# Kernel tuning notes

Measured on AMD Instinct MI355X. Metric: run time of the kernel, lower is better.

## Reference

```python
import jax, jax.numpy as jnp
import numpy as np

LAYERS, H = 12, 8
MH1, MW1 = 32, 32
MH2, MW2 = 63, 63
LENGTHS = [616, 616, 616, 616, 608]  # 2 pairs + tail, sum = L
L = sum(LENGTHS)
N_WITHIN = MH1 * MW1
N_ACROSS = MH2 * MW2
ZERO_SLOT = N_WITHIN + N_ACROSS  # extra table entry that is always 0


def _build_index_maps():
    """Replicates set_indices/_compute_indices/_compute_masks with numpy (static ints)."""
    rng = np.random.default_rng(0)
    rows = rng.integers(0, 31, size=L)
    cols = rng.integers(0, 31, size=L)
    hc2, wc2 = (MH2 - 1) // 2, (MW2 - 1) // 2
    comb = np.full((L, L), ZERO_SLOT, dtype=np.int32)  # untouched cells read 0

    def within_block(r, c):
        hd = np.clip(r[None, :] - r[:, None], 0, MH1 - 1)
        wd = np.clip(c[None, :] - c[:, None], 0, MW1 - 1)
        return (hd * MW1 + wd).astype(np.int32)

    cur = 0
    npairs = len(LENGTHS) // 2
    for i in range(npairs):
        lx, ly = LENGTHS[2 * i], LENGTHS[2 * i + 1]
        xs, xe = cur, cur + lx
        ys, ye = xe, xe + ly
        xr, xc = rows[xs:xe], cols[xs:xe]
        yr, yc = rows[ys:ye], cols[ys:ye]
        comb[xs:xe, xs:xe] = within_block(xr, xc)
        comb[ys:ye, ys:ye] = within_block(yr, yc)
        hdxy = np.clip(yr[:, None] - xr[None, :] + hc2, 0, MH2 - 1)
        wdxy = np.clip(yc[:, None] - xc[None, :] + wc2, 0, MW2 - 1)
        comb[ys:ye, xs:xe] = N_WITHIN + (hdxy * MW2 + wdxy).astype(np.int32)
        cur = ye
    if len(LENGTHS) % 2 == 1:  # tail segment
        lx = LENGTHS[-1]
        xs, xe = cur, cur + lx
        comb[xs:xe, xs:xe] = within_block(rows[xs:xe], cols[xs:xe])

    special = rows == 0
    sp_mask = special[None, :] | special[:, None]
    causal = np.triu(np.ones((L, L), dtype=bool), 1)
    return comb, sp_mask, causal


def setup_inputs() -> dict:
    comb, sp_mask, causal = _build_index_maps()
    key = jax.random.key(0)
    k1, k2 = jax.random.split(key)
    within_bias = jax.random.normal(k1, (LAYERS, H, MH1, MW1), dtype=jnp.float32)
    across_bias = jax.random.normal(k2, (LAYERS, H, MH2, MW2), dtype=jnp.float32)
    return {
        "within_bias": within_bias,
        "across_bias": across_bias,
        "comb_idx": jnp.asarray(comb),
        "sp_mask": jnp.asarray(sp_mask),
        "causal": jnp.asarray(causal),
        "layer_idx": 3,
    }


def reference(within_bias, across_bias, comb_idx, sp_mask, causal, layer_idx):
    h = within_bias.shape[1]
    w = within_bias[layer_idx].reshape(h, -1)           # [H, mh1*mw1]
    a = across_bias[layer_idx].reshape(h, -1)           # [H, mh2*mw2]
    zero = jnp.zeros((h, 1), dtype=w.dtype)
    table = jnp.concatenate([w, a, zero], axis=1)       # [H, nw+na+1]
    attn = table[:, comb_idx]                           # [H, L, L] single gather
    neg = jnp.finfo(attn.dtype).min
    attn = jnp.where(sp_mask, jnp.zeros((), attn.dtype), attn)
    attn = jnp.where(causal, neg, attn)
    return attn[None]                                   # [1, H, L, L]
```

## Files before the change

### kernel.cpp

```cpp
#include <hip/hip_runtime.h>


constexpr int L  = 3072;
constexpr int H  = 8;
constexpr int NW = 32 * 32;
constexpr int NA = 63 * 63;
constexpr int ZERO_SLOT = NW + NA;
constexpr int TBL = ZERO_SLOT + 1;
constexpr unsigned short NEG_F16 = 0xFBFF;
constexpr size_t SPC_OFF = 79936;

typedef __attribute__((ext_vector_type(8))) short short8;

__device__ __forceinline__ unsigned short f16_safe(unsigned short v) {
    return (((v >> 10) & 0x1Fu) == 0x1Fu) ? (unsigned short)0 : v;
}

__global__ __launch_bounds__(256) void mga_prep(
    const unsigned short* __restrict__ within,
    const unsigned short* __restrict__ across,
    const int* __restrict__ layer_idx,
    const unsigned char* __restrict__ sp,
    unsigned short* __restrict__ tbl,
    unsigned char* __restrict__ spc)
{
    const int lw = layer_idx[0];
    const int layer = (lw >= 0 && lw < 12) ? lw : 3;
    const unsigned short* wbase = within + (size_t)layer * H * NW;
    const unsigned short* abase = across + (size_t)layer * H * NA;

    const int t = blockIdx.x * blockDim.x + threadIdx.x;
    if (t < TBL) {
        short8 v;
        #pragma unroll
        for (int h = 0; h < H; ++h) {
            unsigned short x;
            if (t < NW)             x = f16_safe(wbase[h * NW + t]);
            else if (t < ZERO_SLOT) x = f16_safe(abase[h * NA + (t - NW)]);
            else                    x = 0;
            v[h] = (short)x;
        }
        *reinterpret_cast<short8*>(tbl + (size_t)t * H) = v;
    }
    if (t < L) spc[t] = sp[(size_t)t * (L + 1)];
}

__global__ __launch_bounds__(256) void mga_gather(
    const unsigned short* __restrict__ tbl,
    const unsigned char* __restrict__ spc,
    const int*   __restrict__ comb,
    unsigned short* __restrict__ out)
{
    short8 cneg;
    #pragma unroll
    for (int k = 0; k < 8; ++k) cneg[k] = (short)NEG_F16;

    const int g  = blockIdx.x * blockDim.x + threadIdx.x;
    const int e0 = g * 8;
    const int i  = e0 / L;
    const int j  = e0 - i * L;

    unsigned short* o = out + e0;
    if (j > i) {
        #pragma unroll
        for (int h = 0; h < H; ++h)
            *reinterpret_cast<short8*>(o + (size_t)h * (L * L)) = cneg;
        return;
    }

    const int4 ia = *reinterpret_cast<const int4*>(comb + e0);
    const int4 ib = *reinterpret_cast<const int4*>(comb + e0 + 4);
    const unsigned long long spj =
        *reinterpret_cast<const unsigned long long*>(spc + j);
    const bool spi = spc[i] != 0;
    const int idxs[8] = {ia.x, ia.y, ia.z, ia.w, ib.x, ib.y, ib.z, ib.w};

    short8 tt[8];
    bool zm[8], nm[8];
    #pragma unroll
    for (int k = 0; k < 8; ++k) {
        unsigned int idx = (unsigned int)idxs[k];
        idx = (idx > (unsigned)ZERO_SLOT) ? (unsigned)ZERO_SLOT : idx;
        tt[k] = *reinterpret_cast<const short8*>(tbl + (size_t)idx * H);
        zm[k] = spi || (((spj >> (8 * k)) & 1ull) != 0ull);
        nm[k] = (j + k) > i;
    }

    #pragma unroll
    for (int h = 0; h < H; ++h) {
        short8 v;
        #pragma unroll
        for (int k = 0; k < 8; ++k) {
            const unsigned short t =
                nm[k] ? NEG_F16
                      : (zm[k] ? (unsigned short)0 : (unsigned short)tt[k][h]);
            v[k] = (short)t;
        }
        *reinterpret_cast<short8*>(o + (size_t)h * (L * L)) = v;
    }
}

__global__ __launch_bounds__(256) void mga_direct(
    const unsigned short* __restrict__ within,
    const unsigned short* __restrict__ across,
    const int*   __restrict__ comb,
    const unsigned char* __restrict__ sp,
    const int*   __restrict__ layer_idx,
    unsigned short* __restrict__ out)
{
    const int lw = layer_idx[0];
    const int layer = (lw >= 0 && lw < 12) ? lw : 3;
    const unsigned short* wbase = within + (size_t)layer * H * NW;
    const unsigned short* abase = across + (size_t)layer * H * NA;

    const int total  = (L * L) / 8;
    const int stride = gridDim.x * blockDim.x;
    for (int g = blockIdx.x * blockDim.x + threadIdx.x; g < total; g += stride) {
        const int e0 = g * 8;
        const int i  = e0 / L;
        const int j  = e0 - i * L;
        const int4 ia = *reinterpret_cast<const int4*>(comb + e0);
        const int4 ib = *reinterpret_cast<const int4*>(comb + e0 + 4);
        const unsigned long long sp8 =
            *reinterpret_cast<const unsigned long long*>(sp + e0);
        const int idxs[8] = {ia.x, ia.y, ia.z, ia.w, ib.x, ib.y, ib.z, ib.w};
        const unsigned short* p[8];
        int hs[8]; bool zm[8], nm[8];
        #pragma unroll
        for (int k = 0; k < 8; ++k) {
            int idx = idxs[k];
            if (idx < 0 || idx > ZERO_SLOT) idx = ZERO_SLOT;
            const bool isz = (idx >= ZERO_SLOT);
            const bool isw = (idx < NW);
            const unsigned short* pk = isw ? (wbase + idx) : (abase + (idx - NW));
            p[k]  = isz ? wbase : pk;
            hs[k] = isw ? NW : NA;
            zm[k] = isz || (((sp8 >> (8 * k)) & 1ull) != 0ull);
            nm[k] = (j + k) > i;
        }
        unsigned short* o = out + e0;
        #pragma unroll
        for (int h = 0; h < H; ++h) {
            short8 v;
            #pragma unroll
            for (int k = 0; k < 8; ++k) {
                unsigned short t;
                if (nm[k])      t = NEG_F16;
                else if (zm[k]) t = 0;
                else            t = f16_safe(p[k][h * hs[k]]);
                v[k] = (short)t;
            }
            *reinterpret_cast<short8*>(o + (size_t)h * (L * L)) = v;
        }
    }
}

extern "C" void kernel_launch(void* const* d_in, const int* in_sizes, int n_in,
                              void* d_out, int out_size, void* d_ws, size_t ws_size,
                              hipStream_t stream) {
    const unsigned short* within = (const unsigned short*)d_in[0];
    const unsigned short* across = (const unsigned short*)d_in[1];
    const int*   comb   = (const int*)d_in[2];
    const unsigned char* sp = (const unsigned char*)d_in[3];
    const int*   layer  = (const int*)d_in[5];
    unsigned short* out = (unsigned short*)d_out;

    if (ws_size >= SPC_OFF + L) {
        unsigned short* tbl = (unsigned short*)d_ws;
        unsigned char*  spc = (unsigned char*)d_ws + SPC_OFF;
        hipLaunchKernelGGL(mga_prep, dim3((TBL + 255) / 256), dim3(256),
                           0, stream, within, across, layer, sp, tbl, spc);
        hipLaunchKernelGGL(mga_gather, dim3((L * L / 8) / 256), dim3(256),
                           0, stream, tbl, spc, comb, out);
    } else {
        hipLaunchKernelGGL(mga_direct, dim3(2048), dim3(256), 0, stream,
                           within, across, comb, sp, layer, out);
    }
}
```

Measured before the change: 35.00 us.

## Split causal fill into prep kernel and gather only lower-triangle groups

Moves the writing of the strictly-upper-triangle NEG fill into the prep kernel, whose launch now also builds the lookup table, and launches the gather kernel only over 8-element groups on or below the diagonal. Groups are mapped to (row, column) through a closed-form triangular index with a sqrt estimate plus correction loops. This removes the divergent early-exit branch and the warps in the gather kernel that only wrote constants, so the fill can overlap with table construction. The cost is extra integer and sqrt math per thread for the index decode.

```diff
diff --git a/kernel.cpp b/kernel.cpp
--- a/kernel.cpp
+++ b/kernel.cpp
@@ -10,39 +10,72 @@
 constexpr unsigned short NEG_F16 = 0xFBFF;
 constexpr size_t SPC_OFF = 79936;
 
+constexpr int FILL_GROUPS = 588288;
+constexpr int GATH_GROUPS = 591360;
+constexpr int PREP_BLOCKS = 20;
+constexpr int FILL_BLOCKS = FILL_GROUPS / 256;
+constexpr int GATH_BLOCKS = GATH_GROUPS / 256;
+
 typedef __attribute__((ext_vector_type(8))) short short8;
 
 __device__ __forceinline__ unsigned short f16_safe(unsigned short v) {
     return (((v >> 10) & 0x1Fu) == 0x1Fu) ? (unsigned short)0 : v;
 }
 
-__global__ __launch_bounds__(256) void mga_prep(
+__device__ __forceinline__ int cum_fill(int b) { return 3068 * b - 4 * b * b; }
+__device__ __forceinline__ int cum_gath(int b) { return 4 * b * (b + 1); }
+
+__global__ __launch_bounds__(256) void mga_fill_prep(
     const unsigned short* __restrict__ within,
     const unsigned short* __restrict__ across,
     const int* __restrict__ layer_idx,
     const unsigned char* __restrict__ sp,
     unsigned short* __restrict__ tbl,
-    unsigned char* __restrict__ spc)
+    unsigned char* __restrict__ spc,
+    unsigned short* __restrict__ out)
 {
-    const int lw = layer_idx[0];
-    const int layer = (lw >= 0 && lw < 12) ? lw : 3;
-    const unsigned short* wbase = within + (size_t)layer * H * NW;
-    const unsigned short* abase = across + (size_t)layer * H * NA;
-
-    const int t = blockIdx.x * blockDim.x + threadIdx.x;
-    if (t < TBL) {
-        short8 v;
-        #pragma unroll
-        for (int h = 0; h < H; ++h) {
-            unsigned short x;
-            if (t < NW)             x = f16_safe(wbase[h * NW + t]);
-            else if (t < ZERO_SLOT) x = f16_safe(abase[h * NA + (t - NW)]);
-            else                    x = 0;
-            v[h] = (short)x;
-        }
-        *reinterpret_cast<short8*>(tbl + (size_t)t * H) = v;
-    }
-    if (t < L) spc[t] = sp[(size_t)t * (L + 1)];
+    if (blockIdx.x < PREP_BLOCKS) {
+        const int lw = layer_idx[0];
+        const int layer = (lw >= 0 && lw < 12) ? lw : 3;
+        const unsigned short* wbase = within + (size_t)layer * H * NW;
+        const unsigned short* abase = across + (size_t)layer * H * NA;
+        const int t = blockIdx.x * 256 + threadIdx.x;
+        if (t < TBL) {
+            short8 v;
+            #pragma unroll
+            for (int h = 0; h < H; ++h) {
+                unsigned short x;
+                if (t < NW)             x = f16_safe(wbase[h * NW + t]);
+                else if (t < ZERO_SLOT) x = f16_safe(abase[h * NA + (t - NW)]);
+                else                    x = 0;
+                v[h] = (short)x;
+            }
+            *reinterpret_cast<short8*>(tbl + (size_t)t * H) = v;
+        }
+        if (t < L) spc[t] = sp[(size_t)t * (L + 1)];
+        return;
+    }
+
+    const int t = (blockIdx.x - PREP_BLOCKS) * 256 + threadIdx.x;
+    int b = (int)((3068.0f - sqrtf((float)(9412624 - 16 * t))) * 0.125f);
+    b = (b < 0) ? 0 : ((b > 382) ? 382 : b);
+    while (b < 382 && cum_fill(b + 1) <= t) ++b;
+    while (b > 0 && cum_fill(b) > t) --b;
+    const int r8  = t - cum_fill(b);
+    const int cnt = 383 - b;
+    const int r   = r8 / cnt;
+    const int jg  = r8 - r * cnt;
+    const int i   = 8 * b + r;
+    const int j0  = 8 * (b + 1 + jg);
+
+    short8 cneg;
+    #pragma unroll
+    for (int k = 0; k < 8; ++k) cneg[k] = (short)NEG_F16;
+
+    unsigned short* o = out + (size_t)i * L + j0;
+    #pragma unroll
+    for (int h = 0; h < H; ++h)
+        *reinterpret_cast<short8*>(o + (size_t)h * (L * L)) = cneg;
 }
 
 __global__ __launch_bounds__(256) void mga_gather(
@@ -51,27 +84,23 @@
     const int*   __restrict__ comb,
     unsigned short* __restrict__ out)
 {
-    short8 cneg;
-    #pragma unroll
-    for (int k = 0; k < 8; ++k) cneg[k] = (short)NEG_F16;
-
-    const int g  = blockIdx.x * blockDim.x + threadIdx.x;
-    const int e0 = g * 8;
-    const int i  = e0 / L;
-    const int j  = e0 - i * L;
-
-    unsigned short* o = out + e0;
-    if (j > i) {
-        #pragma unroll
-        for (int h = 0; h < H; ++h)
-            *reinterpret_cast<short8*>(o + (size_t)h * (L * L)) = cneg;
-        return;
-    }
+    const int t = blockIdx.x * 256 + threadIdx.x;
+    int b = (int)((sqrtf((float)(t + 1)) - 1.0f) * 0.5f);
+    b = (b < 0) ? 0 : ((b > 383) ? 383 : b);
+    while (b < 383 && cum_gath(b + 1) <= t) ++b;
+    while (b > 0 && cum_gath(b) > t) --b;
+    const int r8  = t - cum_gath(b);
+    const int cnt = b + 1;
+    const int r   = r8 / cnt;
+    const int jg  = r8 - r * cnt;
+    const int i   = 8 * b + r;
+    const int j0  = 8 * jg;
+    const size_t e0 = (size_t)i * L + j0;
 
     const int4 ia = *reinterpret_cast<const int4*>(comb + e0);
     const int4 ib = *reinterpret_cast<const int4*>(comb + e0 + 4);
     const unsigned long long spj =
-        *reinterpret_cast<const unsigned long long*>(spc + j);
+        *reinterpret_cast<const unsigned long long*>(spc + j0);
     const bool spi = spc[i] != 0;
     const int idxs[8] = {ia.x, ia.y, ia.z, ia.w, ib.x, ib.y, ib.z, ib.w};
 
@@ -83,18 +112,19 @@
         idx = (idx > (unsigned)ZERO_SLOT) ? (unsigned)ZERO_SLOT : idx;
         tt[k] = *reinterpret_cast<const short8*>(tbl + (size_t)idx * H);
         zm[k] = spi || (((spj >> (8 * k)) & 1ull) != 0ull);
-        nm[k] = (j + k) > i;
-    }
-
+        nm[k] = (j0 + k) > i;
+    }
+
+    unsigned short* o = out + e0;
     #pragma unroll
     for (int h = 0; h < H; ++h) {
         short8 v;
         #pragma unroll
         for (int k = 0; k < 8; ++k) {
-            const unsigned short t =
+            const unsigned short tv =
                 nm[k] ? NEG_F16
                       : (zm[k] ? (unsigned short)0 : (unsigned short)tt[k][h]);
-            v[k] = (short)t;
+            v[k] = (short)tv;
         }
         *reinterpret_cast<short8*>(o + (size_t)h * (L * L)) = v;
     }
@@ -144,11 +174,11 @@
             short8 v;
             #pragma unroll
             for (int k = 0; k < 8; ++k) {
-                unsigned short t;
-                if (nm[k])      t = NEG_F16;
-                else if (zm[k]) t = 0;
-                else            t = f16_safe(p[k][h * hs[k]]);
-                v[k] = (short)t;
+                unsigned short tv;
+                if (nm[k])      tv = NEG_F16;
+                else if (zm[k]) tv = 0;
+                else            tv = f16_safe(p[k][h * hs[k]]);
+                v[k] = (short)tv;
             }
             *reinterpret_cast<short8*>(o + (size_t)h * (L * L)) = v;
         }
@@ -168,10 +198,11 @@
     if (ws_size >= SPC_OFF + L) {
         unsigned short* tbl = (unsigned short*)d_ws;
         unsigned char*  spc = (unsigned char*)d_ws + SPC_OFF;
-        hipLaunchKernelGGL(mga_prep, dim3((TBL + 255) / 256), dim3(256),
-                           0, stream, within, across, layer, sp, tbl, spc);
-        hipLaunchKernelGGL(mga_gather, dim3((L * L / 8) / 256), dim3(256),
-                           0, stream, tbl, spc, comb, out);
+        hipLaunchKernelGGL(mga_fill_prep, dim3(PREP_BLOCKS + FILL_BLOCKS),
+                           dim3(256), 0, stream,
+                           within, across, layer, sp, tbl, spc, out);
+        hipLaunchKernelGGL(mga_gather, dim3(GATH_BLOCKS), dim3(256), 0, stream,
+                           tbl, spc, comb, out);
     } else {
         hipLaunchKernelGGL(mga_direct, dim3(2048), dim3(256), 0, stream,
                            within, across, comb, sp, layer, out);
```

Result: faster. 33.39 us (-4.6%).
